# Kernel optimization log

Measured on AMD Instinct MI355X. Metric: run time of the kernel, lower is better.

Reference implementation:

```python
import jax, jax.numpy as jnp
import numpy as np

NUM_HEAD = 8  # matches init_kwargs num_head


def setup_inputs() -> dict:
    key = jax.random.key(0)
    ks = jax.random.split(key, 8)
    B, N, C, P = 2, 1024, 512, 256
    cluster_num = 8
    s = 0.02
    return {
        "x_token": jax.random.normal(ks[0], (B, N, C), jnp.float32),
        "x_path": jax.random.normal(ks[1], (B, N, P), jnp.float32),
        "idx_cluster": jax.random.randint(ks[2], (B, N), 0, cluster_num),
        "cluster_num": cluster_num,
        "Wq": jax.random.normal(ks[3], (C, C), jnp.float32) * s,
        "Wk": jax.random.normal(ks[4], (C, C), jnp.float32) * s,
        "Wv": jax.random.normal(ks[5], (C, C), jnp.float32) * s,
        "Wproj": jax.random.normal(ks[6], (C, C), jnp.float32) * s,
        "bproj": jnp.zeros((C,), jnp.float32),
    }


def reference(x_token, x_path, idx_cluster, cluster_num, Wq, Wk, Wv, Wproj, bproj):
    eps = 1e-6
    B, N, C = x_token.shape
    H = NUM_HEAD
    hd = C // H
    scale = hd ** -0.5

    # Linear projections (torch Linear: y = x @ W^T), qkv_bias=False
    q = x_token @ Wq.T
    k = x_token @ Wk.T
    v = (x_token @ Wv.T).reshape(B, N, H, hd).transpose(0, 2, 1, 3)  # (B,H,N,hd)

    qh = q.reshape(B, N, H, hd).transpose(0, 2, 1, 3)  # (B,H,N,hd)
    kh = k.reshape(B, N, H, hd).transpose(0, 2, 1, 3)

    # Raw scaled scores, computed once instead of per-cluster scatter/repeat
    s_ = jnp.einsum('bhid,bhjd->bhij', qh, kh) * scale  # (B,H,N,N)

    # One-hot cluster membership: (B, cluster_num, N)
    m = (idx_cluster[:, None, :] == jnp.arange(cluster_num)[None, :, None]).astype(s_.dtype)

    # attn_map[b,c,h,i,j] = s_[b,h,i,j] if idx[b,i]==c and idx[b,j]==c else 0
    attn_map = s_[:, None] * m[:, :, None, :, None] * m[:, :, None, None, :]  # (B,K,H,N,N)

    # Sum over clusters -> within-cluster scores, zeros elsewhere
    attn = attn_map.sum(axis=1)  # (B,H,N,N)

    # Custom eps-smoothed exp normalization (masked_fill on exact zeros, as in source)
    attn = jnp.where(attn == 0, jnp.float32(-1e9), attn).astype(jnp.float32)
    attn = jnp.exp(attn)
    attn = (attn + eps / N) / (attn.sum(axis=-1, keepdims=True) + eps)

    out = jnp.einsum('bhij,bhjd->bhid', attn, v)  # (B,H,N,hd)
    out = out.transpose(0, 2, 1, 3).reshape(B, N, C)
    out = out @ Wproj.T + bproj
    return out, attn_map
```

## Files before the change

kernel.cpp:

```cpp
#include <hip/hip_runtime.h>
#include <hip/hip_bf16.h>
#include <cstdint>
#include <cstddef>

#define NB   2
#define NN   1024
#define NC   512
#define NH   8
#define NHD  64
#define NK   8

typedef __attribute__((ext_vector_type(8))) short short8v;
typedef __attribute__((ext_vector_type(4))) short short4v;
typedef __attribute__((ext_vector_type(4))) float f32x4;

__device__ __forceinline__ short f2bf(float f) {
    union { float f; unsigned u; } v; v.f = f;
    unsigned r = v.u + 0x7FFFu + ((v.u >> 16) & 1u);
    return (short)(r >> 16);
}

__global__ __launch_bounds__(256) void cast_kernel(
    const float* __restrict__ x, const float* __restrict__ wq,
    const float* __restrict__ wk, const float* __restrict__ wv,
    const float* __restrict__ wp,
    short* __restrict__ xb, short* __restrict__ wqb, short* __restrict__ wkb,
    short* __restrict__ wvb, short* __restrict__ wpb) {
    int i = blockIdx.x * 256 + threadIdx.x;
    if (i < NB * NN * NC) xb[i] = f2bf(x[i]);
    if (i < NC * NC) {
        wqb[i] = f2bf(wq[i]);
        wkb[i] = f2bf(wk[i]);
        wvb[i] = f2bf(wv[i]);
        wpb[i] = f2bf(wp[i]);
    }
}

__global__ __launch_bounds__(256) void qkv_kernel(
    const short* __restrict__ xb, const short* __restrict__ wqb,
    const short* __restrict__ wkb, const short* __restrict__ wvb,
    short* __restrict__ qb, short* __restrict__ kb, short* __restrict__ vT) {
    __shared__ short As[64][40];
    __shared__ short Bs[64][40];
    const int tid = threadIdx.x;
    const int z = blockIdx.z;
    const short* Bsrc = (z == 0) ? wqb : ((z == 1) ? wkb : wvb);
    const int m0 = blockIdx.y * 64, n0 = blockIdx.x * 64;
    const int lane = tid & 63, wave = tid >> 6;
    const int wm = wave >> 1, wn = wave & 1, quad = lane >> 4, lr = lane & 15;
    const int row = tid >> 2, c0 = (tid & 3) * 8;
    f32x4 acc[2][2] = {};
    for (int kt = 0; kt < 512; kt += 32) {
        *(short8v*)&As[row][c0] = *(const short8v*)(xb + (m0 + row) * 512 + kt + c0);
        *(short8v*)&Bs[row][c0] = *(const short8v*)(Bsrc + (n0 + row) * 512 + kt + c0);
        __syncthreads();
        short8v a0 = *(short8v*)&As[wm * 32 + lr][quad * 8];
        short8v a1 = *(short8v*)&As[wm * 32 + 16 + lr][quad * 8];
        short8v b0 = *(short8v*)&Bs[wn * 32 + lr][quad * 8];
        short8v b1 = *(short8v*)&Bs[wn * 32 + 16 + lr][quad * 8];
        acc[0][0] = __builtin_amdgcn_mfma_f32_16x16x32_bf16(a0, b0, acc[0][0], 0, 0, 0);
        acc[0][1] = __builtin_amdgcn_mfma_f32_16x16x32_bf16(a0, b1, acc[0][1], 0, 0, 0);
        acc[1][0] = __builtin_amdgcn_mfma_f32_16x16x32_bf16(a1, b0, acc[1][0], 0, 0, 0);
        acc[1][1] = __builtin_amdgcn_mfma_f32_16x16x32_bf16(a1, b1, acc[1][1], 0, 0, 0);
        __syncthreads();
    }
    for (int sm = 0; sm < 2; sm++)
        for (int sn = 0; sn < 2; sn++)
            for (int r = 0; r < 4; r++) {
                int m = m0 + wm * 32 + sm * 16 + quad * 4 + r;
                int n = n0 + wn * 32 + sn * 16 + lr;
                short v = f2bf(acc[sm][sn][r]);
                if (z == 0) qb[m * 512 + n] = v;
                else if (z == 1) kb[m * 512 + n] = v;
                else {
                    int bb = m >> 10, i = m & 1023, h = n >> 6, d = n & 63;
                    vT[(size_t)(((bb * 8 + h) * 64 + d) << 10) + i] = v;
                }
            }
}

__global__ __launch_bounds__(256) void scores_kernel(
    const short* __restrict__ qb, const short* __restrict__ kb,
    float* __restrict__ attn) {
    __shared__ short As[64][72];
    __shared__ short Bs[64][72];
    const int tid = threadIdx.x;
    const int z = blockIdx.z;
    const int b = z >> 3, h = z & 7;
    const int i0 = blockIdx.y * 64, j0 = blockIdx.x * 64;
    const int lane = tid & 63, wave = tid >> 6;
    const int wm = wave >> 1, wn = wave & 1, quad = lane >> 4, lr = lane & 15;
    {
        int r0 = tid >> 3, cc = (tid & 7) * 8;
        *(short8v*)&As[r0][cc]      = *(const short8v*)(qb + (b * 1024 + i0 + r0) * 512 + h * 64 + cc);
        *(short8v*)&As[r0 + 32][cc] = *(const short8v*)(qb + (b * 1024 + i0 + r0 + 32) * 512 + h * 64 + cc);
        *(short8v*)&Bs[r0][cc]      = *(const short8v*)(kb + (b * 1024 + j0 + r0) * 512 + h * 64 + cc);
        *(short8v*)&Bs[r0 + 32][cc] = *(const short8v*)(kb + (b * 1024 + j0 + r0 + 32) * 512 + h * 64 + cc);
    }
    __syncthreads();
    f32x4 acc[2][2] = {};
    for (int k0 = 0; k0 < 64; k0 += 32) {
        short8v a0 = *(short8v*)&As[wm * 32 + lr][k0 + quad * 8];
        short8v a1 = *(short8v*)&As[wm * 32 + 16 + lr][k0 + quad * 8];
        short8v b0 = *(short8v*)&Bs[wn * 32 + lr][k0 + quad * 8];
        short8v b1 = *(short8v*)&Bs[wn * 32 + 16 + lr][k0 + quad * 8];
        acc[0][0] = __builtin_amdgcn_mfma_f32_16x16x32_bf16(a0, b0, acc[0][0], 0, 0, 0);
        acc[0][1] = __builtin_amdgcn_mfma_f32_16x16x32_bf16(a0, b1, acc[0][1], 0, 0, 0);
        acc[1][0] = __builtin_amdgcn_mfma_f32_16x16x32_bf16(a1, b0, acc[1][0], 0, 0, 0);
        acc[1][1] = __builtin_amdgcn_mfma_f32_16x16x32_bf16(a1, b1, acc[1][1], 0, 0, 0);
    }
    float* srow = attn + ((size_t)(b * 64 + h) << 20);
    for (int sm = 0; sm < 2; sm++)
        for (int sn = 0; sn < 2; sn++)
            for (int r = 0; r < 4; r++) {
                int i = i0 + wm * 32 + sm * 16 + quad * 4 + r;
                int j = j0 + wn * 32 + sn * 16 + lr;
                srow[((size_t)i << 10) + j] = acc[sm][sn][r] * 0.125f;
            }
}

__global__ __launch_bounds__(256) void rowpass_kernel(
    const int* __restrict__ idx, float* __restrict__ attn,
    short* __restrict__ pb) {
    const int tid = threadIdx.x;
    const int bhi = blockIdx.x;
    const int i = bhi & 1023, bh = bhi >> 10, b = bh >> 3, h = bh & 7;
    const int ci = idx[b * 1024 + i];
    const float* srow = attn + (((size_t)(b * 64 + h) << 10) + i) * 1024;
    float4 sv = ((const float4*)srow)[tid];
    int4 iv = ((const int4*)(idx + b * 1024))[tid];
    bool w0 = (iv.x == ci), w1 = (iv.y == ci), w2 = (iv.z == ci), w3 = (iv.w == ci);
    float e0 = (w0 && sv.x != 0.f) ? expf(sv.x) : 0.f;
    float e1 = (w1 && sv.y != 0.f) ? expf(sv.y) : 0.f;
    float e2 = (w2 && sv.z != 0.f) ? expf(sv.z) : 0.f;
    float e3 = (w3 && sv.w != 0.f) ? expf(sv.w) : 0.f;
    __shared__ float red[256];
    red[tid] = e0 + e1 + e2 + e3;
    __syncthreads();
    for (int s = 128; s > 0; s >>= 1) {
        if (tid < s) red[tid] += red[tid + s];
        __syncthreads();
    }
    const float inv = 1.f / (red[0] + 1e-6f);
    const float epsN = 1e-6f / 1024.f;
    short4v pv;
    pv[0] = f2bf((e0 + epsN) * inv);
    pv[1] = f2bf((e1 + epsN) * inv);
    pv[2] = f2bf((e2 + epsN) * inv);
    pv[3] = f2bf((e3 + epsN) * inv);
    *(short4v*)(pb + ((size_t)bhi << 10) + tid * 4) = pv;
    float4 masked;
    masked.x = w0 ? sv.x : 0.f;
    masked.y = w1 ? sv.y : 0.f;
    masked.z = w2 ? sv.z : 0.f;
    masked.w = w3 ? sv.w : 0.f;
    float4 zero4 = {0.f, 0.f, 0.f, 0.f};
    size_t base0 = (((size_t)(b * 64 + h) << 10) + i) * 1024 + tid * 4;
    const size_t cstride = (size_t)8 * 1024 * 1024;
    for (int c = 0; c < 8; c++) {
        float4 wv = (c == ci) ? masked : zero4;
        *(float4*)(attn + base0 + (size_t)c * cstride) = wv;
    }
}

__global__ __launch_bounds__(256) void pv_kernel(
    const short* __restrict__ pb, const short* __restrict__ vT,
    short* __restrict__ oh) {
    __shared__ short As[64][40];
    __shared__ short Bs[64][40];
    const int tid = threadIdx.x;
    const int z = blockIdx.z;
    const int b = z >> 3, h = z & 7;
    const int i0 = blockIdx.y * 64;
    const int lane = tid & 63, wave = tid >> 6;
    const int wm = wave >> 1, wn = wave & 1, quad = lane >> 4, lr = lane & 15;
    const int row = tid >> 2, c0 = (tid & 3) * 8;
    const short* Abase = pb + ((size_t)(z * 1024 + i0) << 10);
    const short* Bbase = vT + ((size_t)z << 16);
    f32x4 acc[2][2] = {};
    for (int kt = 0; kt < 1024; kt += 32) {
        *(short8v*)&As[row][c0] = *(const short8v*)(Abase + ((size_t)row << 10) + kt + c0);
        *(short8v*)&Bs[row][c0] = *(const short8v*)(Bbase + ((size_t)row << 10) + kt + c0);
        __syncthreads();
        short8v a0 = *(short8v*)&As[wm * 32 + lr][quad * 8];
        short8v a1 = *(short8v*)&As[wm * 32 + 16 + lr][quad * 8];
        short8v b0 = *(short8v*)&Bs[wn * 32 + lr][quad * 8];
        short8v b1 = *(short8v*)&Bs[wn * 32 + 16 + lr][quad * 8];
        acc[0][0] = __builtin_amdgcn_mfma_f32_16x16x32_bf16(a0, b0, acc[0][0], 0, 0, 0);
        acc[0][1] = __builtin_amdgcn_mfma_f32_16x16x32_bf16(a0, b1, acc[0][1], 0, 0, 0);
        acc[1][0] = __builtin_amdgcn_mfma_f32_16x16x32_bf16(a1, b0, acc[1][0], 0, 0, 0);
        acc[1][1] = __builtin_amdgcn_mfma_f32_16x16x32_bf16(a1, b1, acc[1][1], 0, 0, 0);
        __syncthreads();
    }
    for (int sm = 0; sm < 2; sm++)
        for (int sn = 0; sn < 2; sn++)
            for (int r = 0; r < 4; r++) {
                int i = i0 + wm * 32 + sm * 16 + quad * 4 + r;
                int d = wn * 32 + sn * 16 + lr;
                oh[((size_t)(b * 1024 + i)) * 512 + h * 64 + d] = f2bf(acc[sm][sn][r]);
            }
}

__global__ __launch_bounds__(256) void proj_kernel(
    const short* __restrict__ oh, const short* __restrict__ wpb,
    const float* __restrict__ bias, float* __restrict__ out) {
    __shared__ short As[64][40];
    __shared__ short Bs[64][40];
    const int tid = threadIdx.x;
    const int m0 = blockIdx.y * 64, n0 = blockIdx.x * 64;
    const int lane = tid & 63, wave = tid >> 6;
    const int wm = wave >> 1, wn = wave & 1, quad = lane >> 4, lr = lane & 15;
    const int row = tid >> 2, c0 = (tid & 3) * 8;
    f32x4 acc[2][2] = {};
    for (int kt = 0; kt < 512; kt += 32) {
        *(short8v*)&As[row][c0] = *(const short8v*)(oh + (m0 + row) * 512 + kt + c0);
        *(short8v*)&Bs[row][c0] = *(const short8v*)(wpb + (n0 + row) * 512 + kt + c0);
        __syncthreads();
        short8v a0 = *(short8v*)&As[wm * 32 + lr][quad * 8];
        short8v a1 = *(short8v*)&As[wm * 32 + 16 + lr][quad * 8];
        short8v b0 = *(short8v*)&Bs[wn * 32 + lr][quad * 8];
        short8v b1 = *(short8v*)&Bs[wn * 32 + 16 + lr][quad * 8];
        acc[0][0] = __builtin_amdgcn_mfma_f32_16x16x32_bf16(a0, b0, acc[0][0], 0, 0, 0);
        acc[0][1] = __builtin_amdgcn_mfma_f32_16x16x32_bf16(a0, b1, acc[0][1], 0, 0, 0);
        acc[1][0] = __builtin_amdgcn_mfma_f32_16x16x32_bf16(a1, b0, acc[1][0], 0, 0, 0);
        acc[1][1] = __builtin_amdgcn_mfma_f32_16x16x32_bf16(a1, b1, acc[1][1], 0, 0, 0);
        __syncthreads();
    }
    for (int sm = 0; sm < 2; sm++)
        for (int sn = 0; sn < 2; sn++)
            for (int r = 0; r < 4; r++) {
                int m = m0 + wm * 32 + sm * 16 + quad * 4 + r;
                int n = n0 + wn * 32 + sn * 16 + lr;
                out[(size_t)m * 512 + n] = acc[sm][sn][r] + bias[n];
            }
}

extern "C" void kernel_launch(void* const* d_in, const int* in_sizes, int n_in,
                              void* d_out, int out_size, void* d_ws, size_t ws_size,
                              hipStream_t stream) {
    const float* x     = (const float*)d_in[0];
    const int*   idx   = (const int*)d_in[2];
    const float* Wq    = (const float*)d_in[4];
    const float* Wk    = (const float*)d_in[5];
    const float* Wv    = (const float*)d_in[6];
    const float* Wp    = (const float*)d_in[7];
    const float* bproj = (const float*)d_in[8];

    float* out  = (float*)d_out;
    float* attn = out + (size_t)NB * NN * NC;

    char* ws = (char*)d_ws;
    short* xb  = (short*)(ws + 0);
    short* wqb = (short*)(ws + 2097152);
    short* wkb = (short*)(ws + 2621440);
    short* wvb = (short*)(ws + 3145728);
    short* wpb = (short*)(ws + 3670016);
    short* qb  = (short*)(ws + 4194304);
    short* kb  = (short*)(ws + 6291456);
    short* vT  = (short*)(ws + 8388608);
    short* oh  = (short*)(ws + 10485760);
    short* pb  = (short*)(ws + 12582912);

    cast_kernel<<<4096, 256, 0, stream>>>(x, Wq, Wk, Wv, Wp, xb, wqb, wkb, wvb, wpb);
    qkv_kernel<<<dim3(8, 32, 3), 256, 0, stream>>>(xb, wqb, wkb, wvb, qb, kb, vT);
    scores_kernel<<<dim3(16, 16, 16), 256, 0, stream>>>(qb, kb, attn);
    rowpass_kernel<<<16384, 256, 0, stream>>>(idx, attn, pb);
    pv_kernel<<<dim3(1, 16, 16), 256, 0, stream>>>(pb, vT, oh);
    proj_kernel<<<dim3(8, 32, 1), 256, 0, stream>>>(oh, wpb, bproj, out);
}
```

Measured before the change: 614.1 us.

## Fuse score masking, exp and attn_map writes into scores kernel; defer normalization

Merges the scores kernel and the row-pass kernel. Each score tile is masked, exponentiated and scattered into the 8-cluster attn_map directly from shared memory using nontemporal stores, so the 64MB fp32 score buffer is no longer written and read back. Row sums are gathered with atomics. Normalization moves into the PV epilogue, which uses the algebraic identity (E·V + eps/N·colsum(V))/rowsum, with colsum computed by a new small kernel. The trade-off is atomics and unnormalized bf16 exponentials, which may change rounding slightly.

```diff
diff --git a/kernel.cpp b/kernel.cpp
--- a/kernel.cpp
+++ b/kernel.cpp
@@ -19,13 +19,19 @@
     unsigned r = v.u + 0x7FFFu + ((v.u >> 16) & 1u);
     return (short)(r >> 16);
 }
+__device__ __forceinline__ float bf2f(short s) {
+    union { unsigned u; float f; } v;
+    v.u = ((unsigned)(unsigned short)s) << 16;
+    return v.f;
+}
 
 __global__ __launch_bounds__(256) void cast_kernel(
     const float* __restrict__ x, const float* __restrict__ wq,
     const float* __restrict__ wk, const float* __restrict__ wv,
     const float* __restrict__ wp,
     short* __restrict__ xb, short* __restrict__ wqb, short* __restrict__ wkb,
-    short* __restrict__ wvb, short* __restrict__ wpb) {
+    short* __restrict__ wvb, short* __restrict__ wpb,
+    float* __restrict__ rowsum) {
     int i = blockIdx.x * 256 + threadIdx.x;
     if (i < NB * NN * NC) xb[i] = f2bf(x[i]);
     if (i < NC * NC) {
@@ -34,6 +40,7 @@
         wvb[i] = f2bf(wv[i]);
         wpb[i] = f2bf(wp[i]);
     }
+    if (i < NB * NH * NN) rowsum[i] = 0.f;
 }
 
 __global__ __launch_bounds__(256) void qkv_kernel(
@@ -79,11 +86,31 @@
             }
 }
 
-__global__ __launch_bounds__(256) void scores_kernel(
+__global__ __launch_bounds__(256) void colsum_kernel(
+    const short* __restrict__ vT, float* __restrict__ colsum) {
+    __shared__ float cp[64][5];
+    const int bh = blockIdx.x, t = threadIdx.x;
+    const int d = t >> 2, seg = t & 3;
+    const short* p = vT + (((size_t)(bh * 64 + d)) << 10) + seg * 256;
+    float s = 0.f;
+    for (int k = 0; k < 256; k += 8) {
+        short8v v = *(const short8v*)(p + k);
+        for (int j = 0; j < 8; j++) s += bf2f(v[j]);
+    }
+    cp[d][seg] = s;
+    __syncthreads();
+    if (t < 64) colsum[bh * 64 + t] = cp[t][0] + cp[t][1] + cp[t][2] + cp[t][3];
+}
+
+__global__ __launch_bounds__(256) void scores_attn_kernel(
     const short* __restrict__ qb, const short* __restrict__ kb,
-    float* __restrict__ attn) {
+    const int* __restrict__ idx, float* __restrict__ attn,
+    short* __restrict__ eb, float* __restrict__ rowsum) {
     __shared__ short As[64][72];
     __shared__ short Bs[64][72];
+    __shared__ float Ss[64][68];
+    __shared__ int idxi[64], idxj[64];
+    __shared__ float rowpart[64][5];
     const int tid = threadIdx.x;
     const int z = blockIdx.z;
     const int b = z >> 3, h = z & 7;
@@ -96,6 +123,8 @@
         *(short8v*)&As[r0 + 32][cc] = *(const short8v*)(qb + (b * 1024 + i0 + r0 + 32) * 512 + h * 64 + cc);
         *(short8v*)&Bs[r0][cc]      = *(const short8v*)(kb + (b * 1024 + j0 + r0) * 512 + h * 64 + cc);
         *(short8v*)&Bs[r0 + 32][cc] = *(const short8v*)(kb + (b * 1024 + j0 + r0 + 32) * 512 + h * 64 + cc);
+        if (tid < 64) idxi[tid] = idx[b * 1024 + i0 + tid];
+        else if (tid < 128) idxj[tid - 64] = idx[b * 1024 + j0 + (tid - 64)];
     }
     __syncthreads();
     f32x4 acc[2][2] = {};
@@ -109,65 +138,53 @@
         acc[1][0] = __builtin_amdgcn_mfma_f32_16x16x32_bf16(a1, b0, acc[1][0], 0, 0, 0);
         acc[1][1] = __builtin_amdgcn_mfma_f32_16x16x32_bf16(a1, b1, acc[1][1], 0, 0, 0);
     }
-    float* srow = attn + ((size_t)(b * 64 + h) << 20);
-    for (int sm = 0; sm < 2; sm++)
-        for (int sn = 0; sn < 2; sn++)
-            for (int r = 0; r < 4; r++) {
-                int i = i0 + wm * 32 + sm * 16 + quad * 4 + r;
-                int j = j0 + wn * 32 + sn * 16 + lr;
-                srow[((size_t)i << 10) + j] = acc[sm][sn][r] * 0.125f;
-            }
-}
-
-__global__ __launch_bounds__(256) void rowpass_kernel(
-    const int* __restrict__ idx, float* __restrict__ attn,
-    short* __restrict__ pb) {
-    const int tid = threadIdx.x;
-    const int bhi = blockIdx.x;
-    const int i = bhi & 1023, bh = bhi >> 10, b = bh >> 3, h = bh & 7;
-    const int ci = idx[b * 1024 + i];
-    const float* srow = attn + (((size_t)(b * 64 + h) << 10) + i) * 1024;
-    float4 sv = ((const float4*)srow)[tid];
-    int4 iv = ((const int4*)(idx + b * 1024))[tid];
-    bool w0 = (iv.x == ci), w1 = (iv.y == ci), w2 = (iv.z == ci), w3 = (iv.w == ci);
-    float e0 = (w0 && sv.x != 0.f) ? expf(sv.x) : 0.f;
-    float e1 = (w1 && sv.y != 0.f) ? expf(sv.y) : 0.f;
-    float e2 = (w2 && sv.z != 0.f) ? expf(sv.z) : 0.f;
-    float e3 = (w3 && sv.w != 0.f) ? expf(sv.w) : 0.f;
-    __shared__ float red[256];
-    red[tid] = e0 + e1 + e2 + e3;
-    __syncthreads();
-    for (int s = 128; s > 0; s >>= 1) {
-        if (tid < s) red[tid] += red[tid + s];
-        __syncthreads();
-    }
-    const float inv = 1.f / (red[0] + 1e-6f);
-    const float epsN = 1e-6f / 1024.f;
-    short4v pv;
-    pv[0] = f2bf((e0 + epsN) * inv);
-    pv[1] = f2bf((e1 + epsN) * inv);
-    pv[2] = f2bf((e2 + epsN) * inv);
-    pv[3] = f2bf((e3 + epsN) * inv);
-    *(short4v*)(pb + ((size_t)bhi << 10) + tid * 4) = pv;
-    float4 masked;
-    masked.x = w0 ? sv.x : 0.f;
-    masked.y = w1 ? sv.y : 0.f;
-    masked.z = w2 ? sv.z : 0.f;
-    masked.w = w3 ? sv.w : 0.f;
-    float4 zero4 = {0.f, 0.f, 0.f, 0.f};
-    size_t base0 = (((size_t)(b * 64 + h) << 10) + i) * 1024 + tid * 4;
-    const size_t cstride = (size_t)8 * 1024 * 1024;
-    for (int c = 0; c < 8; c++) {
-        float4 wv = (c == ci) ? masked : zero4;
-        *(float4*)(attn + base0 + (size_t)c * cstride) = wv;
+    for (int sm = 0; sm < 2; sm++)
+        for (int sn = 0; sn < 2; sn++)
+            for (int r = 0; r < 4; r++)
+                Ss[wm * 32 + sm * 16 + quad * 4 + r][wn * 32 + sn * 16 + lr] = acc[sm][sn][r] * 0.125f;
+    __syncthreads();
+    const int iL = tid >> 2, jb = (tid & 3) * 16;
+    const int ci = idxi[iL];
+    const size_t abase = (((size_t)(b * 64 + h)) << 20) + (((size_t)(i0 + iL)) << 10) + j0 + jb;
+    float rsum = 0.f;
+    short8v e8[2];
+    const f32x4 zero4 = {0.f, 0.f, 0.f, 0.f};
+    for (int chunk = 0; chunk < 4; chunk++) {
+        const int jc = jb + chunk * 4;
+        f32x4 s4 = *(f32x4*)&Ss[iL][jc];
+        f32x4 m4;
+        for (int kk = 0; kk < 4; kk++) {
+            const bool in = (idxj[jc + kk] == ci);
+            const float sv = s4[kk];
+            m4[kk] = in ? sv : 0.f;
+            const float ev = (in && sv != 0.f) ? __expf(sv) : 0.f;
+            rsum += ev;
+            e8[chunk >> 1][(chunk & 1) * 4 + kk] = f2bf(ev);
+        }
+        float* base = attn + abase + chunk * 4;
+        for (int c = 0; c < 8; c++) {
+            f32x4 w = (c == ci) ? m4 : zero4;
+            __builtin_nontemporal_store(w, (f32x4*)(base + ((size_t)c << 23)));
+        }
+    }
+    short* erow = eb + ((((size_t)z << 10) + i0 + iL) << 10) + j0 + jb;
+    *(short8v*)erow = e8[0];
+    *(short8v*)(erow + 8) = e8[1];
+    rowpart[iL][tid & 3] = rsum;
+    __syncthreads();
+    if (tid < 64) {
+        float v = rowpart[tid][0] + rowpart[tid][1] + rowpart[tid][2] + rowpart[tid][3];
+        atomicAdd(&rowsum[(z << 10) + i0 + tid], v);
     }
 }
 
 __global__ __launch_bounds__(256) void pv_kernel(
-    const short* __restrict__ pb, const short* __restrict__ vT,
+    const short* __restrict__ eb, const short* __restrict__ vT,
+    const float* __restrict__ rowsum, const float* __restrict__ colsum,
     short* __restrict__ oh) {
     __shared__ short As[64][40];
     __shared__ short Bs[64][40];
+    __shared__ float invL[64], csL[64];
     const int tid = threadIdx.x;
     const int z = blockIdx.z;
     const int b = z >> 3, h = z & 7;
@@ -175,7 +192,9 @@
     const int lane = tid & 63, wave = tid >> 6;
     const int wm = wave >> 1, wn = wave & 1, quad = lane >> 4, lr = lane & 15;
     const int row = tid >> 2, c0 = (tid & 3) * 8;
-    const short* Abase = pb + ((size_t)(z * 1024 + i0) << 10);
+    if (tid < 64) invL[tid] = 1.f / (rowsum[(z << 10) + i0 + tid] + 1e-6f);
+    else if (tid < 128) csL[tid - 64] = colsum[z * 64 + (tid - 64)];
+    const short* Abase = eb + ((size_t)(z * 1024 + i0) << 10);
     const short* Bbase = vT + ((size_t)z << 16);
     f32x4 acc[2][2] = {};
     for (int kt = 0; kt < 1024; kt += 32) {
@@ -192,12 +211,14 @@
         acc[1][1] = __builtin_amdgcn_mfma_f32_16x16x32_bf16(a1, b1, acc[1][1], 0, 0, 0);
         __syncthreads();
     }
+    const float epsN = 1e-6f / 1024.f;
     for (int sm = 0; sm < 2; sm++)
         for (int sn = 0; sn < 2; sn++)
             for (int r = 0; r < 4; r++) {
-                int i = i0 + wm * 32 + sm * 16 + quad * 4 + r;
+                int iLoc = wm * 32 + sm * 16 + quad * 4 + r;
                 int d = wn * 32 + sn * 16 + lr;
-                oh[((size_t)(b * 1024 + i)) * 512 + h * 64 + d] = f2bf(acc[sm][sn][r]);
+                float val = (acc[sm][sn][r] + epsN * csL[d]) * invL[iLoc];
+                oh[((size_t)(b * 1024 + i0 + iLoc)) * 512 + h * 64 + d] = f2bf(val);
             }
 }
 
@@ -259,12 +280,14 @@
     short* kb  = (short*)(ws + 6291456);
     short* vT  = (short*)(ws + 8388608);
     short* oh  = (short*)(ws + 10485760);
-    short* pb  = (short*)(ws + 12582912);
-
-    cast_kernel<<<4096, 256, 0, stream>>>(x, Wq, Wk, Wv, Wp, xb, wqb, wkb, wvb, wpb);
+    short* eb  = (short*)(ws + 12582912);
+    float* rowsum = (float*)(ws + 46137344);
+    float* colsum = (float*)(ws + 46202880);
+
+    cast_kernel<<<4096, 256, 0, stream>>>(x, Wq, Wk, Wv, Wp, xb, wqb, wkb, wvb, wpb, rowsum);
     qkv_kernel<<<dim3(8, 32, 3), 256, 0, stream>>>(xb, wqb, wkb, wvb, qb, kb, vT);
-    scores_kernel<<<dim3(16, 16, 16), 256, 0, stream>>>(qb, kb, attn);
-    rowpass_kernel<<<16384, 256, 0, stream>>>(idx, attn, pb);
-    pv_kernel<<<dim3(1, 16, 16), 256, 0, stream>>>(pb, vT, oh);
+    colsum_kernel<<<16, 256, 0, stream>>>(vT, colsum);
+    scores_attn_kernel<<<dim3(16, 16, 16), 256, 0, stream>>>(qb, kb, idx, attn, eb, rowsum);
+    pv_kernel<<<dim3(1, 16, 16), 256, 0, stream>>>(eb, vT, rowsum, colsum, oh);
     proj_kernel<<<dim3(8, 32, 1), 256, 0, stream>>>(oh, wpb, bproj, out);
 }
```

After: 1.424 ms. 2.32x slower.
